# Kernel optimization log

Measured on AMD Instinct MI355X. Metric: run time of the kernel, lower is better.

## Reference

```python
import jax, jax.numpy as jnp
import numpy as np

B, T, DM, DH, DD, V, K = 2, 512, 1024, 4096, 4, 32000, 8
THR = 0.25
EPS = 1e-5
IGN = -100


def setup_inputs() -> dict:
    key = jax.random.key(0)
    ks = jax.random.split(key, 12)
    s = 0.02
    return {
        "H": jax.random.normal(ks[0], (B, T, DM), jnp.float32),
        "input_ids": jax.random.randint(ks[1], (B, T), 0, V),
        "attention_mask": jax.random.randint(ks[2], (B, T), 0, 2),
        "labels": jax.random.randint(ks[3], (B, T), 0, V),
        "emb": s * jax.random.normal(ks[4], (V, DM), jnp.float32),
        "depth_emb": s * jax.random.normal(ks[5], (DD, DM), jnp.float32),
        "ln_g": jnp.ones((DM,), jnp.float32),
        "ln_b": jnp.zeros((DM,), jnp.float32),
        "W1": s * jax.random.normal(ks[6], (DM, DH), jnp.float32),
        "b1": jnp.zeros((DH,), jnp.float32),
        "W2": s * jax.random.normal(ks[7], (DH, DM), jnp.float32),
        "b2": jnp.zeros((DM,), jnp.float32),
        "Wq": s * jax.random.normal(ks[8], (DM, V), jnp.float32),
        "bq": jnp.zeros((V,), jnp.float32),
        "Wb": s * jax.random.normal(ks[9], (DM, 1), jnp.float32),
        "bb": jnp.zeros((1,), jnp.float32),
    }


def _forward(H, input_ids, attention_mask, labels, emb, depth_emb, ln_g, ln_b, W1, b1, W2, b2, Wq, bq, Wb, bb):
    mask = attention_mask.astype(bool)  # (B,T)
    E = emb[input_ids]  # (B,T,DM)
    # draft state: broadcast over depth dim
    S = H[:, :, None, :] + E[:, :, None, :] + depth_emb[None, None]  # (B,T,DD,DM)
    mu = S.mean(-1, keepdims=True)
    var = ((S - mu) ** 2).mean(-1, keepdims=True)  # biased var, as torch LayerNorm
    S = (S - mu) * jax.lax.rsqrt(var + EPS) * ln_g + ln_b
    S = jax.nn.gelu(S @ W1 + b1, approximate=False) @ W2 + b2
    q = S @ Wq + bq  # (B,T,DD,V)
    beta = (S @ Wb + bb)[..., 0]  # (B,T,DD)
    q = jnp.where(mask[:, :, None, None], q, 0.0)
    beta = jnp.where(mask[:, :, None], beta, 0.0)
    # future labels for D depths (small fixed loop over DD)
    targets = jnp.full((B, T, DD), IGN, jnp.int32)
    valid = jnp.zeros((B, T, DD), bool)
    for d in range(1, DD + 1):
        v = mask[:, : T - d] & mask[:, d:]
        valid = valid.at[:, : T - d, d - 1].set(v)
        targets = targets.at[:, : T - d, d - 1].set(
            jnp.where(v, labels[:, d:].astype(jnp.int32), IGN))
    # token CE over valid positions (masked mean)
    logp = jax.nn.log_softmax(q, axis=-1)
    safe = jnp.where(valid, targets, 0)
    nll = -jnp.take_along_axis(logp, safe[..., None], axis=-1)[..., 0]
    cnt = valid.sum()
    L_q = jnp.where(cnt > 0, (nll * valid).sum() / jnp.maximum(cnt, 1).astype(q.dtype), jnp.zeros((), q.dtype))
    # BCE-with-logits on beta, averaged over valid source positions
    bce = jnp.logaddexp(0.0, beta) - beta * valid.astype(beta.dtype)
    src = valid.any(-1, keepdims=True)
    denom = jnp.maximum(src.sum(), 1).astype(beta.dtype)
    L_beta = (bce * src).sum() / denom
    return q, beta, L_q + L_beta


def reference(H, input_ids, attention_mask, labels, emb, depth_emb, ln_g, ln_b, W1, b1, W2, b2, Wq, bq, Wb, bb):
    q, beta, loss = _forward(H, input_ids, attention_mask, labels, emb, depth_emb,
                             ln_g, ln_b, W1, b1, W2, b2, Wq, bq, Wb, bb)
    # dynamic_branch_width
    sigma = jax.nn.sigmoid(beta)
    k = jnp.clip(jnp.ceil(sigma * float(K)).astype(jnp.int32), 1, K)
    k = jnp.where(sigma >= THR, k, 0)
    k = jnp.where(attention_mask.astype(bool)[:, :, None], k, 0)
    return q, beta, k, loss
```

## Files before the change

kernel.cpp:

```cpp
#include <hip/hip_runtime.h>
#include <math.h>

#define B_ 2
#define T_ 512
#define DM_ 1024
#define DH_ 4096
#define DD_ 4
#define V_ 32000
#define M_ 4096
#define BT_ 1024
#define NCHUNK3_ 125
#define PCH_ 128

typedef __attribute__((ext_vector_type(8))) unsigned short ushort8_t;
typedef __attribute__((ext_vector_type(4))) unsigned short ushort4_t;
typedef __attribute__((ext_vector_type(8))) __bf16 bf16x8;
typedef __attribute__((ext_vector_type(4))) float f32x4;

__device__ __forceinline__ unsigned short f2bf(float x) {
  union { float f; unsigned u; } v; v.f = x;
  unsigned r = v.u + 0x7fffu + ((v.u >> 16) & 1u);
  return (unsigned short)(r >> 16);
}
__device__ __forceinline__ float bf2f(unsigned short h) {
  union { unsigned u; float f; } v; v.u = ((unsigned)h) << 16; return v.f;
}

__device__ __forceinline__ void gload16(const void* g, void* l) {
  __builtin_amdgcn_global_load_lds(
      (const __attribute__((address_space(1))) void*)g,
      (__attribute__((address_space(3))) void*)l, 16, 0, 0);
}

template<int ROWS, int NWAVE>
__device__ __forceinline__ void stage_swz(const unsigned short* __restrict__ src, int ld,
                                          unsigned short* lds, int wid, int lane) {
  constexpr int NLOAD = ROWS / (16 * NWAVE);
  const int rl = lane >> 2;
  const int slot = (lane & 3) ^ ((lane >> 3) & 3);
  #pragma unroll
  for (int i = 0; i < NLOAD; ++i) {
    const int rbase = (i * NWAVE + wid) * 16;
    gload16(src + (size_t)(rbase + rl) * ld + slot * 8, lds + rbase * 32);
  }
}

__device__ __forceinline__ bf16x8 ldfrag(const unsigned short* t, int r, int s) {
  return __builtin_bit_cast(bf16x8,
      *(const ushort8_t*)&t[r * 32 + ((s ^ ((r >> 1) & 3)) * 8)]);
}

__device__ __forceinline__ float block_sum256(float v, float* sh) {
  #pragma unroll
  for (int o = 32; o >= 1; o >>= 1) v += __shfl_down(v, o);
  int lane = threadIdx.x & 63, wid = threadIdx.x >> 6;
  if (lane == 0) sh[wid] = v;
  __syncthreads();
  float t = sh[0] + sh[1] + sh[2] + sh[3];
  __syncthreads();
  return t;
}

__global__ __launch_bounds__(256) void transpose_split_kernel(
    const float* __restrict__ in, int R, int C,
    unsigned short* __restrict__ out_hi, unsigned short* __restrict__ out_lo)
{
  __shared__ float tile[32][33];
  int c0 = blockIdx.x * 32, r0 = blockIdx.y * 32;
  int tx = threadIdx.x & 31, ty = threadIdx.x >> 5;
  #pragma unroll
  for (int i = 0; i < 4; ++i)
    tile[ty + i * 8][tx] = in[(size_t)(r0 + ty + i * 8) * C + c0 + tx];
  __syncthreads();
  #pragma unroll
  for (int i = 0; i < 4; ++i) {
    int orow = c0 + ty + i * 8;
    int ocol = r0 + tx;
    float v = tile[tx][ty + i * 8];
    unsigned short h = f2bf(v);
    out_hi[(size_t)orow * R + ocol] = h;
    if (out_lo) out_lo[(size_t)orow * R + ocol] = f2bf(v - bf2f(h));
  }
}

__global__ __launch_bounds__(256) void embed_ln_kernel(
    const float* __restrict__ H, const int* __restrict__ ids,
    const float* __restrict__ emb, const float* __restrict__ demb,
    const float* __restrict__ g, const float* __restrict__ be,
    unsigned short* __restrict__ Xhi, unsigned short* __restrict__ Xlo)
{
  __shared__ float sh[8];
  int m = blockIdx.x, tid = threadIdx.x;
  int bt = m >> 2, d = m & 3;
  int id = ids[bt];
  float4 x  = ((const float4*)(H   + (size_t)bt * DM_))[tid];
  float4 e  = ((const float4*)(emb + (size_t)id * DM_))[tid];
  float4 de = ((const float4*)(demb + (size_t)d * DM_))[tid];
  float v0 = x.x + e.x + de.x, v1 = x.y + e.y + de.y;
  float v2 = x.z + e.z + de.z, v3 = x.w + e.w + de.w;
  float mu = block_sum256((v0 + v1) + (v2 + v3), sh) * (1.0f / DM_);
  float d0 = v0 - mu, d1v = v1 - mu, d2 = v2 - mu, d3 = v3 - mu;
  float var = block_sum256((d0 * d0 + d1v * d1v) + (d2 * d2 + d3 * d3), sh) * (1.0f / DM_);
  float rs = rsqrtf(var + 1e-5f);
  float4 gg  = ((const float4*)g)[tid];
  float4 bb4 = ((const float4*)be)[tid];
  float y0 = d0 * rs * gg.x + bb4.x;
  float y1 = d1v * rs * gg.y + bb4.y;
  float y2 = d2 * rs * gg.z + bb4.z;
  float y3 = d3 * rs * gg.w + bb4.w;
  unsigned short h0 = f2bf(y0), h1 = f2bf(y1), h2 = f2bf(y2), h3 = f2bf(y3);
  ushort4_t hv = {h0, h1, h2, h3};
  ushort4_t lv = {f2bf(y0 - bf2f(h0)), f2bf(y1 - bf2f(h1)), f2bf(y2 - bf2f(h2)), f2bf(y3 - bf2f(h3))};
  size_t base = (size_t)m * DM_ + tid * 4;
  *(ushort4_t*)&Xhi[base] = hv;
  *(ushort4_t*)&Xlo[base] = lv;
}

__global__ __launch_bounds__(64) void w2b_kernel(
    const float* __restrict__ W2, const float* __restrict__ Wb,
    const float* __restrict__ b2, const float* __restrict__ bb,
    float* __restrict__ w2b)
{
  int j = blockIdx.x, lane = threadIdx.x;
  const float* rowp = (j < DH_) ? (W2 + (size_t)j * DM_) : b2;
  const float4* r4 = (const float4*)rowp;
  const float4* w4 = (const float4*)Wb;
  float s = 0.0f;
  for (int i = lane; i < DM_ / 4; i += 64) {
    float4 a = r4[i], w = w4[i];
    s += a.x * w.x + a.y * w.y + a.z * w.z + a.w * w.w;
  }
  #pragma unroll
  for (int o = 32; o >= 1; o >>= 1) s += __shfl_down(s, o);
  if (lane == 0) w2b[j] = (j < DH_) ? s : (s + bb[0]);
}

template<int BM, int BN, int NWAVE, int WN,
         bool SPLIT, bool GELU, bool CEPART, bool BETAPART, bool NTC>
__global__ __launch_bounds__(NWAVE * 64, 2) void gemm2p_kernel(
    const unsigned short* __restrict__ Ahi, const unsigned short* __restrict__ Alo,
    const unsigned short* __restrict__ Bhi, const unsigned short* __restrict__ Blo,
    const float* __restrict__ bias, int Ndim, int Kdim,
    float* __restrict__ Cf, unsigned short* __restrict__ Chi, unsigned short* __restrict__ Clo,
    const int* __restrict__ rowmask,
    const float* __restrict__ w2bv, float* __restrict__ bpart,
    float* __restrict__ pmax, float* __restrict__ psum)
{
  constexpr int WM = NWAVE / WN;
  constexpr int MI = (BM / WM) / 16;
  constexpr int NI = (BN / WN) / 16;
  constexpr int AW = BM * 32;
  constexpr int BW = BN * 32;
  constexpr int BUFW = (SPLIT ? 2 : 1) * (AW + BW);
  __shared__ __align__(16) unsigned short smem[2 * BUFW];

  const int m0 = blockIdx.x * BM, n0 = blockIdx.y * BN;
  const int tid = threadIdx.x, lane = tid & 63, wid = tid >> 6;
  const int wr = wid / WN, wc = wid % WN;
  const int lrow = lane & 15, q4 = lane >> 4;
  const int wrb = wr * (BM / WM), wcb = wc * (BN / WN);

  const unsigned short* Ab  = Ahi + (size_t)m0 * Kdim;
  const unsigned short* Bb  = Bhi + (size_t)n0 * Kdim;
  const unsigned short* Alb = SPLIT ? (Alo + (size_t)m0 * Kdim) : nullptr;
  const unsigned short* Blb = SPLIT ? (Blo + (size_t)n0 * Kdim) : nullptr;

  f32x4 acc[MI][NI] = {};
  const int NT = Kdim / 32;

  auto stageAll = [&](int buf, int kt) {
    unsigned short* base = smem + buf * BUFW;
    const int ko = kt * 32;
    stage_swz<BM, NWAVE>(Ab + ko, Kdim, base, wid, lane);
    stage_swz<BN, NWAVE>(Bb + ko, Kdim, base + AW, wid, lane);
    if constexpr (SPLIT) {
      stage_swz<BM, NWAVE>(Alb + ko, Kdim, base + AW + BW, wid, lane);
      stage_swz<BN, NWAVE>(Blb + ko, Kdim, base + 2 * AW + BW, wid, lane);
    }
  };

  stageAll(0, 0);
  asm volatile("s_waitcnt vmcnt(0)" ::: "memory");
  __syncthreads();

  int cur = 0;
  for (int kt = 0; kt < NT; ++kt) {
    if (kt + 1 < NT) stageAll(cur ^ 1, kt + 1);
    __builtin_amdgcn_sched_barrier(0);
    const unsigned short* sA = smem + cur * BUFW;
    const unsigned short* sB = sA + AW;
    bf16x8 bh[NI], bl[NI];
    #pragma unroll
    for (int ni = 0; ni < NI; ++ni) {
      bh[ni] = ldfrag(sB, wcb + ni * 16 + lrow, q4);
      if constexpr (SPLIT) bl[ni] = ldfrag(sB + AW + BW, wcb + ni * 16 + lrow, q4);
    }
    #pragma unroll
    for (int mi = 0; mi < MI; ++mi) {
      const int r = wrb + mi * 16 + lrow;
      bf16x8 ah = ldfrag(sA, r, q4);
      bf16x8 al;
      if constexpr (SPLIT) al = ldfrag(sA + AW + BW, r, q4);
      #pragma unroll
      for (int ni = 0; ni < NI; ++ni) {
        acc[mi][ni] = __builtin_amdgcn_mfma_f32_16x16x32_bf16(ah, bh[ni], acc[mi][ni], 0, 0, 0);
        if constexpr (SPLIT) {
          acc[mi][ni] = __builtin_amdgcn_mfma_f32_16x16x32_bf16(ah, bl[ni], acc[mi][ni], 0, 0, 0);
          acc[mi][ni] = __builtin_amdgcn_mfma_f32_16x16x32_bf16(al, bh[ni], acc[mi][ni], 0, 0, 0);
        }
      }
    }
    asm volatile("s_waitcnt vmcnt(0)" ::: "memory");
    __syncthreads();
    cur ^= 1;
  }

  #pragma unroll
  for (int mi = 0; mi < MI; ++mi)
    #pragma unroll
    for (int ni = 0; ni < NI; ++ni) {
      const int col = n0 + wcb + ni * 16 + lrow;
      const float bv = bias ? bias[col] : 0.0f;
      #pragma unroll
      for (int r2 = 0; r2 < 4; ++r2) {
        const int gm = m0 + wrb + mi * 16 + q4 * 4 + r2;
        float v = acc[mi][ni][r2] + bv;
        if constexpr (GELU) v = 0.5f * v * (1.0f + erff(v * 0.70710678118654752440f));
        if (rowmask) v *= (rowmask[gm >> 2] ? 1.0f : 0.0f);
        acc[mi][ni][r2] = v;
        const size_t idx = (size_t)gm * Ndim + col;
        if (Cf) {
          if constexpr (NTC) __builtin_nontemporal_store(v, &Cf[idx]);
          else Cf[idx] = v;
        }
        if (Chi) {
          unsigned short h = f2bf(v);
          Chi[idx] = h;
          if (Clo) Clo[idx] = f2bf(v - bf2f(h));
        }
      }
    }

  float* red = (float*)smem;

  if constexpr (CEPART) {
    #pragma unroll
    for (int mi = 0; mi < MI; ++mi)
      #pragma unroll
      for (int r2 = 0; r2 < 4; ++r2) {
        float mx = -3.4e38f;
        #pragma unroll
        for (int ni = 0; ni < NI; ++ni) mx = fmaxf(mx, acc[mi][ni][r2]);
        #pragma unroll
        for (int o = 1; o < 16; o <<= 1) mx = fmaxf(mx, __shfl_xor(mx, o));
        float sm = 0.0f;
        #pragma unroll
        for (int ni = 0; ni < NI; ++ni) sm += expf(acc[mi][ni][r2] - mx);
        #pragma unroll
        for (int o = 1; o < 16; o <<= 1) sm += __shfl_xor(sm, o);
        if (lrow == 0) {
          const int rowL = wrb + mi * 16 + q4 * 4 + r2;
          red[(rowL * WN + wc) * 2 + 0] = mx;
          red[(rowL * WN + wc) * 2 + 1] = sm;
        }
      }
    __syncthreads();
    for (int r = tid; r < BM; r += NWAVE * 64) {
      float mg = -3.4e38f, sg = 0.0f;
      #pragma unroll
      for (int w = 0; w < WN; ++w) {
        float mw = red[(r * WN + w) * 2 + 0], sw = red[(r * WN + w) * 2 + 1];
        float nm = fmaxf(mg, mw);
        sg = sg * expf(mg - nm) + sw * expf(mw - nm);
        mg = nm;
      }
      pmax[(size_t)(m0 + r) * PCH_ + blockIdx.y] = mg;
      psum[(size_t)(m0 + r) * PCH_ + blockIdx.y] = sg;
    }
  }

  if constexpr (BETAPART) {
    #pragma unroll
    for (int mi = 0; mi < MI; ++mi)
      #pragma unroll
      for (int r2 = 0; r2 < 4; ++r2) {
        float s = 0.0f;
        #pragma unroll
        for (int ni = 0; ni < NI; ++ni)
          s += acc[mi][ni][r2] * w2bv[n0 + wcb + ni * 16 + lrow];
        #pragma unroll
        for (int o = 1; o < 16; o <<= 1) s += __shfl_xor(s, o);
        if (lrow == 0)
          red[(wrb + mi * 16 + q4 * 4 + r2) * WN + wc] = s;
      }
    __syncthreads();
    for (int r = tid; r < BM; r += NWAVE * 64) {
      float s = 0.0f;
      #pragma unroll
      for (int w = 0; w < WN; ++w) s += red[r * WN + w];
      bpart[(size_t)(m0 + r) * 32 + blockIdx.y] = s;
    }
  }
}

__global__ __launch_bounds__(64) void beta_k_kernel(
    const float* __restrict__ bpart, const float* __restrict__ w2b,
    const int* __restrict__ mask,
    float* __restrict__ beta_out, float* __restrict__ k_out,
    float* __restrict__ bce, int* __restrict__ validf)
{
  int m = blockIdx.x, lane = threadIdx.x;
  float s = (lane < 32) ? bpart[(size_t)m * 32 + lane] : 0.0f;
  #pragma unroll
  for (int o = 32; o >= 1; o >>= 1) s += __shfl_down(s, o);
  if (lane == 0) {
    int bt = m >> 2, d1 = (m & 3) + 1;
    float beta = s + w2b[DH_];
    int mv = mask[bt];
    float bm = mv ? beta : 0.0f;
    int t = bt % T_;
    int valid = (t + d1 < T_) && mv && mask[bt + d1];
    beta_out[m] = bm;
    float sp = fmaxf(bm, 0.0f) + log1pf(expf(-fabsf(bm)));
    bce[m] = sp - (valid ? bm : 0.0f);
    validf[m] = valid;
    float sig = 1.0f / (1.0f + expf(-bm));
    int kk = (int)ceilf(sig * 8.0f);
    kk = kk < 1 ? 1 : (kk > 8 ? 8 : kk);
    if (!(sig >= 0.25f)) kk = 0;
    if (!mv) kk = 0;
    k_out[m] = (float)kk;
  }
}

__global__ __launch_bounds__(64) void ce_reduce_kernel(
    const float* __restrict__ pmax, const float* __restrict__ psum,
    const float* __restrict__ q, const int* __restrict__ validf,
    const int* __restrict__ labels, float* __restrict__ nll)
{
  int m = blockIdx.x, lane = threadIdx.x;
  if (!validf[m]) { if (lane == 0) nll[m] = 0.0f; return; }
  float ml = -3.4e38f, sl = 0.0f;
  for (int j = lane; j < NCHUNK3_; j += 64) {
    float mj = pmax[(size_t)m * PCH_ + j], sj = psum[(size_t)m * PCH_ + j];
    float nm = fmaxf(ml, mj);
    sl = sl * expf(ml - nm) + sj * expf(mj - nm);
    ml = nm;
  }
  #pragma unroll
  for (int o = 32; o >= 1; o >>= 1) {
    float mo = __shfl_xor(ml, o), so = __shfl_xor(sl, o);
    float nm = fmaxf(ml, mo);
    sl = sl * expf(ml - nm) + so * expf(mo - nm);
    ml = nm;
  }
  if (lane == 0) {
    int bt = m >> 2, d1 = (m & 3) + 1;
    float qt = q[(size_t)m * V_ + labels[bt + d1]];
    nll[m] = -(qt - ml - logf(sl));
  }
}

__global__ __launch_bounds__(256) void loss_kernel(
    const float* __restrict__ nll, const int* __restrict__ validf,
    const float* __restrict__ bce, float* __restrict__ loss_out)
{
  __shared__ float sh[8];
  int tid = threadIdx.x;
  float snll = 0.0f, fcnt = 0.0f, sbce = 0.0f, fnsrc = 0.0f;
  for (int m = tid; m < M_; m += 256) { snll += nll[m]; fcnt += (float)validf[m]; }
  for (int bt = tid; bt < BT_; bt += 256) {
    int base = bt * 4;
    int src = validf[base] | validf[base + 1] | validf[base + 2] | validf[base + 3];
    if (src) { sbce += bce[base] + bce[base + 1] + bce[base + 2] + bce[base + 3]; fnsrc += 1.0f; }
  }
  snll = block_sum256(snll, sh);
  fcnt = block_sum256(fcnt, sh);
  sbce = block_sum256(sbce, sh);
  fnsrc = block_sum256(fnsrc, sh);
  if (tid == 0) {
    float Lq = fcnt > 0.0f ? snll / fcnt : 0.0f;
    float Lb = sbce / fmaxf(fnsrc, 1.0f);
    loss_out[0] = Lq + Lb;
  }
}

extern "C" void kernel_launch(void* const* d_in, const int* in_sizes, int n_in,
                              void* d_out, int out_size, void* d_ws, size_t ws_size,
                              hipStream_t stream) {
  const float* H    = (const float*)d_in[0];
  const int*   ids  = (const int*)d_in[1];
  const int*   mask = (const int*)d_in[2];
  const int*   labels = (const int*)d_in[3];
  const float* emb  = (const float*)d_in[4];
  const float* demb = (const float*)d_in[5];
  const float* ln_g = (const float*)d_in[6];
  const float* ln_b = (const float*)d_in[7];
  const float* W1   = (const float*)d_in[8];
  const float* b1   = (const float*)d_in[9];
  const float* W2   = (const float*)d_in[10];
  const float* b2   = (const float*)d_in[11];
  const float* Wq   = (const float*)d_in[12];
  const float* bq   = (const float*)d_in[13];
  const float* Wb   = (const float*)d_in[14];
  const float* bb   = (const float*)d_in[15];

  char* ws = (char*)d_ws; size_t off = 0;
  auto walloc = [&](size_t bytes) -> void* {
    void* p = ws + off; off = (off + bytes + 255) & ~(size_t)255; return p;
  };
  unsigned short* W1t_hi = (unsigned short*)walloc((size_t)DH_ * DM_ * 2);
  unsigned short* W1t_lo = (unsigned short*)walloc((size_t)DH_ * DM_ * 2);
  unsigned short* W2t_hi = (unsigned short*)walloc((size_t)DM_ * DH_ * 2);
  unsigned short* Wqt_hi = (unsigned short*)walloc((size_t)V_ * DM_ * 2);
  unsigned short* Xhi    = (unsigned short*)walloc((size_t)M_ * DM_ * 2);
  unsigned short* Xlo    = (unsigned short*)walloc((size_t)M_ * DM_ * 2);
  unsigned short* S2hi   = (unsigned short*)walloc((size_t)M_ * DM_ * 2);
  float* w2b    = (float*)walloc((DH_ + 1) * 4);
  float* bpart  = (float*)walloc((size_t)M_ * 32 * 4);
  float* pmax   = (float*)walloc((size_t)M_ * PCH_ * 4);
  float* psum   = (float*)walloc((size_t)M_ * PCH_ * 4);
  float* nll    = (float*)walloc(M_ * 4);
  float* bcev   = (float*)walloc(M_ * 4);
  int*   validf = (int*)walloc(M_ * 4);

  float* q_out    = (float*)d_out;
  float* beta_out = q_out + (size_t)M_ * V_;
  float* k_out    = beta_out + M_;
  float* loss_out = k_out + M_;
  unsigned short* act_hi = (unsigned short*)d_out;
  unsigned short* act_lo = act_hi + (size_t)M_ * DH_;

  transpose_split_kernel<<<dim3(DH_ / 32, DM_ / 32), 256, 0, stream>>>(W1, DM_, DH_, W1t_hi, W1t_lo);
  transpose_split_kernel<<<dim3(DM_ / 32, DH_ / 32), 256, 0, stream>>>(W2, DH_, DM_, W2t_hi, nullptr);
  transpose_split_kernel<<<dim3(V_ / 32, DM_ / 32), 256, 0, stream>>>(Wq, DM_, V_, Wqt_hi, nullptr);
  embed_ln_kernel<<<M_, 256, 0, stream>>>(H, ids, emb, demb, ln_g, ln_b, Xhi, Xlo);
  w2b_kernel<<<DH_ + 1, 64, 0, stream>>>(W2, Wb, b2, bb, w2b);
  gemm2p_kernel<128, 128, 8, 4, true, true, false, true, false>
      <<<dim3(M_ / 128, DH_ / 128), 512, 0, stream>>>(
      Xhi, Xlo, W1t_hi, W1t_lo, b1, DH_, DM_, nullptr, act_hi, act_lo, nullptr,
      w2b, bpart, nullptr, nullptr);
  beta_k_kernel<<<M_, 64, 0, stream>>>(bpart, w2b, mask, beta_out, k_out, bcev, validf);
  gemm2p_kernel<128, 128, 4, 2, false, false, false, false, false>
      <<<dim3(M_ / 128, DM_ / 128), 256, 0, stream>>>(
      act_hi, nullptr, W2t_hi, nullptr, b2, DM_, DH_, nullptr, S2hi, nullptr, nullptr,
      nullptr, nullptr, nullptr, nullptr);
  gemm2p_kernel<256, 256, 8, 4, false, false, true, false, true>
      <<<dim3(M_ / 256, V_ / 256), 512, 0, stream>>>(
      S2hi, nullptr, Wqt_hi, nullptr, bq, V_, DM_, q_out, nullptr, nullptr, mask,
      nullptr, nullptr, pmax, psum);
  ce_reduce_kernel<<<M_, 64, 0, stream>>>(pmax, psum, q_out, validf, labels, nll);
  loss_kernel<<<1, 256, 0, stream>>>(nll, validf, bcev, loss_out);
}
```

Baseline: 1.497 ms.

## Triple-buffer LDS staging in GEMM kernels with a single barrier per k-step

Switches the shared GEMM template from double to triple buffering of LDS tiles. It prefetches two k-tiles ahead, waits on partial vmcnt(4) instead of draining all loads, and uses one barrier per iteration instead of two. The aim is to hide global-load latency behind MFMA work. Shared memory per block grows by half, to about 96KB for the 256x256 and split 128x128 variants. That likely limits those GEMMs to one resident block per CU and cuts occupancy.

```diff
diff --git a/kernel.cpp b/kernel.cpp
--- a/kernel.cpp
+++ b/kernel.cpp
@@ -137,7 +137,7 @@
 
 template<int BM, int BN, int NWAVE, int WN,
          bool SPLIT, bool GELU, bool CEPART, bool BETAPART, bool NTC>
-__global__ __launch_bounds__(NWAVE * 64, 2) void gemm2p_kernel(
+__global__ __launch_bounds__(NWAVE * 64, 2) void gemm3p_kernel(
     const unsigned short* __restrict__ Ahi, const unsigned short* __restrict__ Alo,
     const unsigned short* __restrict__ Bhi, const unsigned short* __restrict__ Blo,
     const float* __restrict__ bias, int Ndim, int Kdim,
@@ -152,7 +152,9 @@
   constexpr int AW = BM * 32;
   constexpr int BW = BN * 32;
   constexpr int BUFW = (SPLIT ? 2 : 1) * (AW + BW);
-  __shared__ __align__(16) unsigned short smem[2 * BUFW];
+  constexpr int LPS = (SPLIT ? 2 : 1) * (BM / (16 * NWAVE) + BN / (16 * NWAVE));
+  static_assert(LPS == 4, "vmcnt(4) assumes exactly 4 loads per wave per stage");
+  __shared__ __align__(16) unsigned short smem[3 * BUFW];
 
   const int m0 = blockIdx.x * BM, n0 = blockIdx.y * BN;
   const int tid = threadIdx.x, lane = tid & 63, wid = tid >> 6;
@@ -168,8 +170,7 @@
   f32x4 acc[MI][NI] = {};
   const int NT = Kdim / 32;
 
-  auto stageAll = [&](int buf, int kt) {
-    unsigned short* base = smem + buf * BUFW;
+  auto stageAll = [&](unsigned short* base, int kt) {
     const int ko = kt * 32;
     stage_swz<BM, NWAVE>(Ab + ko, Kdim, base, wid, lane);
     stage_swz<BN, NWAVE>(Bb + ko, Kdim, base + AW, wid, lane);
@@ -179,16 +180,23 @@
     }
   };
 
-  stageAll(0, 0);
-  asm volatile("s_waitcnt vmcnt(0)" ::: "memory");
-  __syncthreads();
-
-  int cur = 0;
+  unsigned short* p0 = smem;
+  unsigned short* p1 = smem + BUFW;
+  unsigned short* p2 = smem + 2 * BUFW;
+
+  stageAll(p0, 0);
+  stageAll(p1, 1);
+
   for (int kt = 0; kt < NT; ++kt) {
-    if (kt + 1 < NT) stageAll(cur ^ 1, kt + 1);
+    if (kt + 1 < NT) asm volatile("s_waitcnt vmcnt(4)" ::: "memory");
+    else             asm volatile("s_waitcnt vmcnt(0)" ::: "memory");
+    __builtin_amdgcn_s_barrier();
     __builtin_amdgcn_sched_barrier(0);
-    const unsigned short* sA = smem + cur * BUFW;
-    const unsigned short* sB = sA + AW;
+    if (kt + 2 < NT) stageAll(p2, kt + 2);
+    __builtin_amdgcn_sched_barrier(0);
+
+    const unsigned short* sA = p0;
+    const unsigned short* sB = p0 + AW;
     bf16x8 bh[NI], bl[NI];
     #pragma unroll
     for (int ni = 0; ni < NI; ++ni) {
@@ -210,10 +218,9 @@
         }
       }
     }
-    asm volatile("s_waitcnt vmcnt(0)" ::: "memory");
-    __syncthreads();
-    cur ^= 1;
-  }
+    unsigned short* t = p0; p0 = p1; p1 = p2; p2 = t;
+  }
+  __syncthreads();
 
   #pragma unroll
   for (int mi = 0; mi < MI; ++mi)
@@ -436,16 +443,16 @@
   transpose_split_kernel<<<dim3(V_ / 32, DM_ / 32), 256, 0, stream>>>(Wq, DM_, V_, Wqt_hi, nullptr);
   embed_ln_kernel<<<M_, 256, 0, stream>>>(H, ids, emb, demb, ln_g, ln_b, Xhi, Xlo);
   w2b_kernel<<<DH_ + 1, 64, 0, stream>>>(W2, Wb, b2, bb, w2b);
-  gemm2p_kernel<128, 128, 8, 4, true, true, false, true, false>
+  gemm3p_kernel<128, 128, 8, 4, true, true, false, true, false>
       <<<dim3(M_ / 128, DH_ / 128), 512, 0, stream>>>(
       Xhi, Xlo, W1t_hi, W1t_lo, b1, DH_, DM_, nullptr, act_hi, act_lo, nullptr,
       w2b, bpart, nullptr, nullptr);
   beta_k_kernel<<<M_, 64, 0, stream>>>(bpart, w2b, mask, beta_out, k_out, bcev, validf);
-  gemm2p_kernel<128, 128, 4, 2, false, false, false, false, false>
+  gemm3p_kernel<128, 128, 4, 2, false, false, false, false, false>
       <<<dim3(M_ / 128, DM_ / 128), 256, 0, stream>>>(
       act_hi, nullptr, W2t_hi, nullptr, b2, DM_, DH_, nullptr, S2hi, nullptr, nullptr,
       nullptr, nullptr, nullptr, nullptr);
-  gemm2p_kernel<256, 256, 8, 4, false, false, true, false, true>
+  gemm3p_kernel<256, 256, 8, 4, false, false, true, false, true>
       <<<dim3(M_ / 256, V_ / 256), 512, 0, stream>>>(
       S2hi, nullptr, Wqt_hi, nullptr, bq, V_, DM_, q_out, nullptr, nullptr, mask,
       nullptr, nullptr, pmax, psum);
```

Measured after the change: 1.392 ms. 1.08x faster.
